# Performance work log

Measured on AMD Instinct MI355X. Metric: run time of the kernel, lower is better.

Reference implementation:

```python
import jax, jax.numpy as jnp
import numpy as np
from jax import lax

B = 128      # graphs per batch
N = 68       # facial landmarks (num_nodes per graph)
C = 3        # input channels
P = 32       # PATCH_SIZE
K = 16       # NUM_KERNELS
FD = 64      # feature_dim
GH = 128     # gcn_hidden_dim
OUT = 2      # output_dim
EG = 8 * N   # edges per graph
T = B * N    # total nodes


def setup_inputs() -> dict:
    key = jax.random.key(0)
    ks = jax.random.split(key, 8)
    x = jax.random.normal(ks[0], (T, C, P, P), jnp.float32)
    e = jax.random.randint(ks[1], (2, B, EG), 0, N)
    offs = (jnp.arange(B) * N)[None, :, None]
    edge_index = (e + offs).reshape(2, -1)            # within-graph edges, global ids
    batch = jnp.repeat(jnp.arange(B), N)              # node -> graph id
    conv_w = jax.random.normal(ks[2], (N, K, C, 3, 3), jnp.float32) * 0.05
    conv_b = jnp.zeros((N, K), jnp.float32)
    lin1_w = jax.random.normal(ks[3], (N, K * (P // 2) * (P // 2), FD), jnp.float32) * 0.02
    lin1_b = jnp.zeros((N, FD), jnp.float32)
    gcn_w = jax.random.normal(ks[4], (FD, GH), jnp.float32) * 0.1
    gcn_b = jnp.zeros((GH,), jnp.float32)
    mlp_w1 = jax.random.normal(ks[5], (GH, GH // 2), jnp.float32) * 0.1
    mlp_b1 = jnp.zeros((GH // 2,), jnp.float32)
    mlp_w2 = jax.random.normal(ks[6], (GH // 2, OUT), jnp.float32) * 0.1
    mlp_b2 = jnp.zeros((OUT,), jnp.float32)
    return dict(x=x, edge_index=edge_index, batch=batch, conv_w=conv_w, conv_b=conv_b,
                lin1_w=lin1_w, lin1_b=lin1_b, gcn_w=gcn_w, gcn_b=gcn_b,
                mlp_w1=mlp_w1, mlp_b1=mlp_b1, mlp_w2=mlp_w2, mlp_b2=mlp_b2)


def reference(x, edge_index, batch, conv_w, conv_b, lin1_w, lin1_b,
              gcn_w, gcn_b, mlp_w1, mlp_b1, mlp_w2, mlp_b2):
    # --- per-node-type CNN routing (nodes are laid out [graph, local_index]) ---
    xr = x.reshape(B, N, C, P, P)

    def cnn_one(xn, w, b):           # xn: [B,C,P,P]  w: [K,C,3,3]
        y = lax.conv_general_dilated(xn, w, (1, 1), 'SAME',
                                     dimension_numbers=('NCHW', 'OIHW', 'NCHW'))
        return jax.nn.relu(y + b[None, :, None, None])

    a = jax.vmap(cnn_one, in_axes=(1, 0, 0), out_axes=1)(xr, conv_w, conv_b)  # [B,N,K,P,P]
    pooled = lax.reduce_window(a, -jnp.inf, lax.max,
                               (1, 1, 1, 2, 2), (1, 1, 1, 2, 2), 'VALID')     # [B,N,K,P/2,P/2]
    flat = pooled.reshape(B, N, -1)
    feats = jax.nn.relu(jnp.einsum('bnf,nfo->bno', flat, lin1_w) + lin1_b[None])  # [B,N,FD]
    nodes = feats.reshape(T, FD)

    # --- GCNConv: add self-loops, symmetric normalization ---
    loop = jnp.arange(T)
    src = jnp.concatenate([edge_index[0], loop])
    dst = jnp.concatenate([edge_index[1], loop])
    deg = jax.ops.segment_sum(jnp.ones_like(dst, jnp.float32), dst, T)
    dis = jnp.where(deg > 0, 1.0 / jnp.sqrt(deg), 0.0)
    norm = dis[src] * dis[dst]
    xw = nodes @ gcn_w                                   # [T,GH]
    h = jax.ops.segment_sum(norm[:, None] * xw[src], dst, T) + gcn_b
    h = jax.nn.relu(h)

    # --- global mean pool over graphs ---
    cnt = jax.ops.segment_sum(jnp.ones((T,), jnp.float32), batch, B)
    g = jax.ops.segment_sum(h, batch, B) / cnt[:, None]  # [B,GH]

    # --- MLP head ---
    z = jax.nn.relu(g @ mlp_w1 + mlp_b1)
    return z @ mlp_w2 + mlp_b2                           # [B,OUT]
```

## Files before the change

### kernel.cpp

```cpp
#include <hip/hip_runtime.h>
#include <hip/hip_fp16.h>

#define B_   128
#define N_   68
#define C_   3
#define P_   32
#define K_   16
#define FD_  64
#define GH_  128
#define EG_  544
#define T_   8704
#define FLAT_ 4096
#define FCH_ 16

typedef __attribute__((ext_vector_type(8))) _Float16 half8;
typedef __attribute__((ext_vector_type(2))) _Float16 half2v;
typedef __attribute__((ext_vector_type(4))) float   floatx4;
typedef __attribute__((ext_vector_type(4))) unsigned int uint32x4;

#define XPITCH 1164

__global__ __launch_bounds__(256) void conv_pool_kernel(
    const float* __restrict__ x, const float* __restrict__ conv_w,
    const float* __restrict__ conv_b, _Float16* __restrict__ pooled) {
  const int t = blockIdx.x;
  const int n = t % N_;
  const int tid = threadIdx.x;

  __shared__ _Float16 xsh[3 * XPITCH];
  __shared__ __align__(16) _Float16 wAS[2][16][32];
  __shared__ __align__(16) _Float16 wCS[2][16][32];
  __shared__ __align__(16) float bS[16];

  const float* wp = conv_w + (size_t)n * (K_ * 27);

  for (int i = tid; i < 1024; i += 256) {
    int sx = i >> 9, k = (i >> 5) & 15, slot = i & 31;
    int q = slot >> 3, r = (slot >> 2) & 1, col = slot & 3;
    int cr = q * 2 + r, c = cr / 3, dy = cr - c * 3, dx = col - sx;
    float v = (dx >= 0 && dx < 3) ? wp[k * 27 + c * 9 + dy * 3 + dx] : 0.0f;
    wAS[sx][k][slot] = (_Float16)v;
  }
  for (int i = tid; i < 1024; i += 256) {
    int sx = i >> 9, k = (i >> 5) & 15, slot = i & 31;
    int q = slot >> 3, j = slot & 7;
    float v = 0.0f;
    if (q == 0 && j < 4) {
      int dx = j - sx;
      if (dx >= 0 && dx < 3) v = wp[k * 27 + 2 * 9 + 2 * 3 + dx];
    }
    wCS[sx][k][slot] = (_Float16)v;
  }
  if (tid < 16) bS[tid] = conv_b[(size_t)n * K_ + tid];

  for (int i = tid; i < 396; i += 256) {
    int c = i / 132, j = i - c * 132;
    int off;
    if (j < 34)       off = j;
    else if (j < 68)  off = 33 * 34 + (j - 34);
    else if (j < 100) off = (j - 68 + 1) * 34;
    else              off = (j - 100 + 1) * 34 + 33;
    xsh[c * XPITCH + off] = (_Float16)0.0f;
  }
  const float4* xg = (const float4*)(x + (size_t)t * (C_ * P_ * P_));
  #pragma unroll
  for (int j = 0; j < 3; j++) {
    int i4 = tid + j * 256;
    float4 v = xg[i4];
    int f0 = i4 * 4;
    int c = f0 >> 10, rem = f0 & 1023, y = rem >> 5, xc = rem & 31;
    _Float16* dp = &xsh[c * XPITCH + (y + 1) * 34 + xc + 1];
    dp[0] = (_Float16)v.x; dp[1] = (_Float16)v.y;
    dp[2] = (_Float16)v.z; dp[3] = (_Float16)v.w;
  }
  __syncthreads();

  const int lane = tid & 63, wave = tid >> 6;
  const int lr = lane & 15, q = lane >> 4;
  const int ldy = lr >> 3, ldx = lr & 7;

  half8 aMain0 = *(const half8*)&wAS[0][lr][q * 8];
  half8 aMain1 = *(const half8*)&wAS[1][lr][q * 8];
  half8 aCorr0 = *(const half8*)&wCS[0][lr][q * 8];
  half8 aCorr1 = *(const half8*)&wCS[1][lr][q * 8];
  floatx4 cbias = *(const floatx4*)&bS[q * 4];

  const int crL = q * 2, crH = crL + 1;
  const int cL = crL / 3, dyL = crL - cL * 3;
  const int cH = crH / 3, dyH = crH - cH * 3;
  const _Float16* chL = &xsh[cL * XPITCH + dyL * 34];
  const _Float16* chH = &xsh[cH * XPITCH + dyH * 34];
  const _Float16* chC = &xsh[2 * XPITCH + 2 * 34];

  #pragma unroll
  for (int i = 0; i < 4; i++) {
    const int qq = wave * 4 + i;
    const int py0 = (qq >> 1) * 2, px0 = (qq & 1) * 8;
    const int py = py0 + ldy, px = px0 + ldx;
    const int ebase = py * 68 + px * 2;
    const _Float16* pL = chL + ebase;
    const _Float16* pH = chH + ebase;
    const _Float16* pC = chC + ebase;

    floatx4 mx;
    #pragma unroll
    for (int sy = 0; sy < 2; sy++) {
      unsigned int uL0 = *(const unsigned int*)&pL[sy * 34];
      unsigned int uL1 = *(const unsigned int*)&pL[sy * 34 + 2];
      unsigned int uH0 = *(const unsigned int*)&pH[sy * 34];
      unsigned int uH1 = *(const unsigned int*)&pH[sy * 34 + 2];
      unsigned int uC0 = *(const unsigned int*)&pC[sy * 34];
      unsigned int uC1 = *(const unsigned int*)&pC[sy * 34 + 2];
      half8 bMain = __builtin_bit_cast(half8, (uint32x4){uL0, uL1, uH0, uH1});
      half8 bCorr = __builtin_bit_cast(half8, (uint32x4){uC0, uC1, uC0, uC1});
      floatx4 d0 = __builtin_amdgcn_mfma_f32_16x16x32_f16(aCorr0, bCorr, cbias, 0, 0, 0);
      d0 = __builtin_amdgcn_mfma_f32_16x16x32_f16(aMain0, bMain, d0, 0, 0, 0);
      floatx4 d1 = __builtin_amdgcn_mfma_f32_16x16x32_f16(aCorr1, bCorr, cbias, 0, 0, 0);
      d1 = __builtin_amdgcn_mfma_f32_16x16x32_f16(aMain1, bMain, d1, 0, 0, 0);
      floatx4 m;
      m[0] = fmaxf(d0[0], d1[0]); m[1] = fmaxf(d0[1], d1[1]);
      m[2] = fmaxf(d0[2], d1[2]); m[3] = fmaxf(d0[3], d1[3]);
      if (sy == 0) mx = m;
      else {
        mx[0] = fmaxf(mx[0], m[0]); mx[1] = fmaxf(mx[1], m[1]);
        mx[2] = fmaxf(mx[2], m[2]); mx[3] = fmaxf(mx[3], m[3]);
      }
    }
    _Float16* op = pooled + (size_t)t * FLAT_ + q * 1024 + py * 16 + px;
    op[0]   = (_Float16)fmaxf(mx[0], 0.0f);
    op[256] = (_Float16)fmaxf(mx[1], 0.0f);
    op[512] = (_Float16)fmaxf(mx[2], 0.0f);
    op[768] = (_Float16)fmaxf(mx[3], 0.0f);
  }
}

__global__ __launch_bounds__(256) void lin1_mfma_kernel(
    const _Float16* __restrict__ pooled, const float* __restrict__ lin1_w,
    float* __restrict__ part) {
  const int n   = blockIdx.x >> 4;
  const int fc  = blockIdx.x & 15;
  const int tid = threadIdx.x;
  const int wave = tid >> 6, lane = tid & 63;
  const int q = lane >> 4, lr = lane & 15;

  __shared__ __align__(16) _Float16 As[128 * 72];
  __shared__ __align__(16) _Float16 Bt[64 * 72];

  floatx4 acc[2][4];
  #pragma unroll
  for (int mt = 0; mt < 2; mt++)
    #pragma unroll
    for (int nt = 0; nt < 4; nt++)
      acc[mt][nt] = (floatx4){0.f, 0.f, 0.f, 0.f};

  const int f_base = fc * 256;
  for (int step = 0; step < 4; step++) {
    const int f0 = f_base + step * 64;

    #pragma unroll
    for (int j = 0; j < 4; j++) {
      int idx = tid + j * 256;
      int r = idx >> 3, ch = idx & 7;
      uint4 v = *(const uint4*)&pooled[(size_t)(r * N_ + n) * FLAT_ + f0 + ch * 8];
      *(uint4*)&As[r * 72 + ch * 8] = v;
    }
    const float* wg = &lin1_w[(size_t)n * (FLAT_ * FD_) + (size_t)f0 * FD_];
    #pragma unroll
    for (int it = 0; it < 2; it++) {
      int p = tid + it * 256;
      int o0 = (p & 15) * 4, k0 = (p >> 4) * 2;
      const float* wgk = wg + k0 * 64 + o0;
      float4 va = *(const float4*)wgk;
      float4 vb = *(const float4*)(wgk + 64);
      *(half2v*)&Bt[(o0 + 0) * 72 + k0] = (half2v){(_Float16)va.x, (_Float16)vb.x};
      *(half2v*)&Bt[(o0 + 1) * 72 + k0] = (half2v){(_Float16)va.y, (_Float16)vb.y};
      *(half2v*)&Bt[(o0 + 2) * 72 + k0] = (half2v){(_Float16)va.z, (_Float16)vb.z};
      *(half2v*)&Bt[(o0 + 3) * 72 + k0] = (half2v){(_Float16)va.w, (_Float16)vb.w};
    }
    __syncthreads();

    #pragma unroll
    for (int kh = 0; kh < 2; kh++) {
      half8 af[2], bf[4];
      #pragma unroll
      for (int mt = 0; mt < 2; mt++)
        af[mt] = *(const half8*)&As[(wave * 32 + mt * 16 + lr) * 72 + kh * 32 + q * 8];
      #pragma unroll
      for (int nt = 0; nt < 4; nt++)
        bf[nt] = *(const half8*)&Bt[(nt * 16 + lr) * 72 + kh * 32 + q * 8];
      #pragma unroll
      for (int mt = 0; mt < 2; mt++)
        #pragma unroll
        for (int nt = 0; nt < 4; nt++)
          acc[mt][nt] = __builtin_amdgcn_mfma_f32_16x16x32_f16(
              af[mt], bf[nt], acc[mt][nt], 0, 0, 0);
    }
    __syncthreads();
  }

  float* pb = part + (size_t)fc * T_ * FD_;
  #pragma unroll
  for (int mt = 0; mt < 2; mt++) {
    #pragma unroll
    for (int v = 0; v < 4; v++) {
      int r = wave * 32 + mt * 16 + q * 4 + v;
      size_t base = (size_t)(r * N_ + n) * FD_;
      #pragma unroll
      for (int nt = 0; nt < 4; nt++)
        pb[base + nt * 16 + lr] = acc[mt][nt][v];
    }
  }
}

__global__ __launch_bounds__(256) void feats_kernel(
    const float* __restrict__ part, const float* __restrict__ lin1_b,
    float* __restrict__ feats) {
  int gid = blockIdx.x * 256 + threadIdx.x;
  int t = gid >> 4, f4 = (gid & 15) * 4;
  int n = t % N_;
  float4 s = *(const float4*)&lin1_b[n * FD_ + f4];
  #pragma unroll
  for (int fc = 0; fc < FCH_; fc++) {
    float4 v = *(const float4*)&part[((size_t)fc * T_ + t) * FD_ + f4];
    s.x += v.x; s.y += v.y; s.z += v.z; s.w += v.w;
  }
  s.x = fmaxf(s.x, 0.f); s.y = fmaxf(s.y, 0.f);
  s.z = fmaxf(s.z, 0.f); s.w = fmaxf(s.w, 0.f);
  *(float4*)&feats[(size_t)t * FD_ + f4] = s;
}

__global__ __launch_bounds__(256) void gcn_agg_kernel(
    const float* __restrict__ feats, const int* __restrict__ edge_index,
    float* __restrict__ agg) {
  const int b  = blockIdx.x >> 1;
  const int fh = blockIdx.x & 1;
  const int tid = threadIdx.x;

  __shared__ float fS[N_ * 33], aS[N_ * 33];
  __shared__ int   esrcS[EG_], edstS[EG_];
  __shared__ float nrmS[EG_];
  __shared__ int   degS[N_];
  __shared__ float disS[N_];

  if (tid < N_) degS[tid] = 0;
  const int* srcp = edge_index;
  const int* dstp = edge_index + (B_ * EG_);
  const int e0 = b * EG_, nbase = b * N_;
  for (int e = tid; e < EG_; e += 256) {
    esrcS[e] = srcp[e0 + e] - nbase;
    edstS[e] = dstp[e0 + e] - nbase;
  }
  for (int idx = tid; idx < N_ * 32; idx += 256) {
    int i = idx >> 5, f = idx & 31;
    fS[i * 33 + f] = feats[(size_t)(b * N_ + i) * FD_ + fh * 32 + f];
  }
  __syncthreads();
  for (int e = tid; e < EG_; e += 256) atomicAdd(&degS[edstS[e]], 1);
  __syncthreads();
  if (tid < N_) disS[tid] = rsqrtf((float)(degS[tid] + 1));
  __syncthreads();
  for (int e = tid; e < EG_; e += 256)
    nrmS[e] = disS[esrcS[e]] * disS[edstS[e]];
  for (int idx = tid; idx < N_ * 32; idx += 256) {
    int i = idx >> 5, f = idx & 31;
    float d = disS[i];
    aS[i * 33 + f] = d * d * fS[i * 33 + f];
  }
  __syncthreads();
  for (int idx = tid; idx < EG_ * 32; idx += 256) {
    int e = idx >> 5, f = idx & 31;
    atomicAdd(&aS[edstS[e] * 33 + f], nrmS[e] * fS[esrcS[e] * 33 + f]);
  }
  __syncthreads();
  for (int idx = tid; idx < N_ * 32; idx += 256) {
    int i = idx >> 5, f = idx & 31;
    agg[(size_t)(b * N_ + i) * FD_ + fh * 32 + f] = aS[i * 33 + f];
  }
}

__global__ __launch_bounds__(512) void gcn_head_kernel(
    const float* __restrict__ agg, const float* __restrict__ gcn_w,
    const float* __restrict__ gcn_b, const float* __restrict__ w1,
    const float* __restrict__ b1, const float* __restrict__ w2,
    const float* __restrict__ b2, float* __restrict__ out) {
  const int b = blockIdx.x;
  const int tid = threadIdx.x;

  __shared__ float aS[N_ * 68];
  __shared__ float wS[FD_ * GH_];
  __shared__ float gP[4][GH_];
  __shared__ float z1S[64];

  for (int i4 = tid; i4 < N_ * 16; i4 += 512) {
    int i = i4 >> 4, qf = (i4 & 15) * 4;
    *(float4*)&aS[i * 68 + qf] = *(const float4*)&agg[(size_t)(b * N_ + i) * FD_ + qf];
  }
  #pragma unroll
  for (int j = 0; j < 4; j++)
    ((float4*)wS)[tid + j * 512] = ((const float4*)gcn_w)[tid + j * 512];
  __syncthreads();

  const int j = tid & 127, ig = tid >> 7;
  float wc[64];
  #pragma unroll
  for (int k = 0; k < 64; k++) wc[k] = wS[k * GH_ + j];
  const float bias = gcn_b[j];
  float gsum = 0.f;
  for (int i = ig; i < N_; i += 4) {
    float acc = bias;
    #pragma unroll
    for (int kq = 0; kq < 16; kq++) {
      float4 a = *(const float4*)&aS[i * 68 + kq * 4];
      acc += a.x * wc[kq * 4] + a.y * wc[kq * 4 + 1]
           + a.z * wc[kq * 4 + 2] + a.w * wc[kq * 4 + 3];
    }
    gsum += fmaxf(acc, 0.f);
  }
  gP[ig][j] = gsum;
  __syncthreads();
  if (tid < GH_)
    gP[0][tid] = (gP[0][tid] + gP[1][tid] + gP[2][tid] + gP[3][tid]) * (1.f / 68.f);
  __syncthreads();
  if (tid < 64) {
    float s = b1[tid];
    #pragma unroll 8
    for (int jj = 0; jj < GH_; jj++) s += gP[0][jj] * w1[jj * 64 + tid];
    z1S[tid] = fmaxf(s, 0.f);
  }
  __syncthreads();
  if (tid < 2) {
    float s = b2[tid];
    #pragma unroll 8
    for (int jj = 0; jj < 64; jj++) s += z1S[jj] * w2[jj * 2 + tid];
    out[b * 2 + tid] = s;
  }
}

extern "C" void kernel_launch(void* const* d_in, const int* in_sizes, int n_in,
                              void* d_out, int out_size, void* d_ws, size_t ws_size,
                              hipStream_t stream) {
  const float* x        = (const float*)d_in[0];
  const int*   edge_idx = (const int*)d_in[1];
  const float* conv_w   = (const float*)d_in[3];
  const float* conv_b   = (const float*)d_in[4];
  const float* lin1_w   = (const float*)d_in[5];
  const float* lin1_b   = (const float*)d_in[6];
  const float* gcn_w    = (const float*)d_in[7];
  const float* gcn_b    = (const float*)d_in[8];
  const float* mlp_w1   = (const float*)d_in[9];
  const float* mlp_b1   = (const float*)d_in[10];
  const float* mlp_w2   = (const float*)d_in[11];
  const float* mlp_b2   = (const float*)d_in[12];
  float* outp = (float*)d_out;

  char* wsb = (char*)d_ws;
  _Float16* pooled = (_Float16*)wsb;
  float* part  = (float*)(wsb + (size_t)T_ * FLAT_ * 2);
  float* feats = part + (size_t)FCH_ * T_ * FD_;
  float* agg   = feats + (size_t)T_ * FD_;

  conv_pool_kernel<<<T_, 256, 0, stream>>>(x, conv_w, conv_b, pooled);
  lin1_mfma_kernel<<<N_ * FCH_, 256, 0, stream>>>(pooled, lin1_w, part);
  feats_kernel<<<544, 256, 0, stream>>>(part, lin1_b, feats);
  gcn_agg_kernel<<<B_ * 2, 256, 0, stream>>>(feats, edge_idx, agg);
  gcn_head_kernel<<<B_, 512, 0, stream>>>(agg, gcn_w, gcn_b,
                                          mlp_w1, mlp_b1, mlp_w2, mlp_b2, outp);
}
```

Measured before the change: 315.3 us.

## Precompute conv weight fragments once per node type and pad LDS rows

```diff
diff --git a/kernel.cpp b/kernel.cpp
--- a/kernel.cpp
+++ b/kernel.cpp
@@ -18,86 +18,94 @@
 typedef __attribute__((ext_vector_type(4))) float   floatx4;
 typedef __attribute__((ext_vector_type(4))) unsigned int uint32x4;
 
-#define XPITCH 1164
+#define ROWP 40
+#define CHP  1400
+
+__global__ __launch_bounds__(256) void wfrag_prep_kernel(
+    const float* __restrict__ conv_w, _Float16* __restrict__ wfrag) {
+  const int n = blockIdx.x;
+  const int tid = threadIdx.x;
+  const float* wp = conv_w + (size_t)n * (K_ * 27);
+  _Float16* out = wfrag + (size_t)n * 2048;
+  for (int i = tid; i < 2048; i += 256) {
+    int sx   = (i >> 10) & 1;
+    int type = (i >> 9) & 1;
+    int k    = (i >> 5) & 15;
+    int slot = i & 31;
+    float v = 0.0f;
+    if (type == 0) {
+      int q = slot >> 3, r = (slot >> 2) & 1, col = slot & 3;
+      int cr = q * 2 + r, c = cr / 3, dy = cr - c * 3, dx = col - sx;
+      if (dx >= 0 && dx < 3) v = wp[k * 27 + c * 9 + dy * 3 + dx];
+    } else {
+      int q = slot >> 3, j = slot & 7;
+      if (q == 0 && j < 4) {
+        int dx = j - sx;
+        if (dx >= 0 && dx < 3) v = wp[k * 27 + 24 + dx];
+      }
+    }
+    out[i] = (_Float16)v;
+  }
+}
 
 __global__ __launch_bounds__(256) void conv_pool_kernel(
-    const float* __restrict__ x, const float* __restrict__ conv_w,
+    const float* __restrict__ x, const _Float16* __restrict__ wfrag,
     const float* __restrict__ conv_b, _Float16* __restrict__ pooled) {
   const int t = blockIdx.x;
   const int n = t % N_;
   const int tid = threadIdx.x;
 
-  __shared__ _Float16 xsh[3 * XPITCH];
-  __shared__ __align__(16) _Float16 wAS[2][16][32];
-  __shared__ __align__(16) _Float16 wCS[2][16][32];
-  __shared__ __align__(16) float bS[16];
-
-  const float* wp = conv_w + (size_t)n * (K_ * 27);
-
-  for (int i = tid; i < 1024; i += 256) {
-    int sx = i >> 9, k = (i >> 5) & 15, slot = i & 31;
-    int q = slot >> 3, r = (slot >> 2) & 1, col = slot & 3;
-    int cr = q * 2 + r, c = cr / 3, dy = cr - c * 3, dx = col - sx;
-    float v = (dx >= 0 && dx < 3) ? wp[k * 27 + c * 9 + dy * 3 + dx] : 0.0f;
-    wAS[sx][k][slot] = (_Float16)v;
-  }
-  for (int i = tid; i < 1024; i += 256) {
-    int sx = i >> 9, k = (i >> 5) & 15, slot = i & 31;
-    int q = slot >> 3, j = slot & 7;
-    float v = 0.0f;
-    if (q == 0 && j < 4) {
-      int dx = j - sx;
-      if (dx >= 0 && dx < 3) v = wp[k * 27 + 2 * 9 + 2 * 3 + dx];
-    }
-    wCS[sx][k][slot] = (_Float16)v;
-  }
-  if (tid < 16) bS[tid] = conv_b[(size_t)n * K_ + tid];
+  __shared__ _Float16 xsh[3 * CHP];
+
+  const int lane = tid & 63;
+  const int lr = lane & 15, q = lane >> 4;
+  const int wave = tid >> 6;
+  const int ldy = lr >> 3, ldx = lr & 7;
+
+  const float4* xg = (const float4*)(x + (size_t)t * (C_ * P_ * P_));
+  float4 xv[3];
+  #pragma unroll
+  for (int j = 0; j < 3; j++) xv[j] = xg[tid + j * 256];
+
+  const _Float16* wf = wfrag + (size_t)n * 2048 + lr * 32 + q * 8;
+  half8 aMain0 = *(const half8*)&wf[0 * 512];
+  half8 aCorr0 = *(const half8*)&wf[1 * 512];
+  half8 aMain1 = *(const half8*)&wf[2 * 512];
+  half8 aCorr1 = *(const half8*)&wf[3 * 512];
+  floatx4 cbias = *(const floatx4*)&conv_b[(size_t)n * K_ + q * 4];
 
   for (int i = tid; i < 396; i += 256) {
     int c = i / 132, j = i - c * 132;
     int off;
     if (j < 34)       off = j;
-    else if (j < 68)  off = 33 * 34 + (j - 34);
-    else if (j < 100) off = (j - 68 + 1) * 34;
-    else              off = (j - 100 + 1) * 34 + 33;
-    xsh[c * XPITCH + off] = (_Float16)0.0f;
-  }
-  const float4* xg = (const float4*)(x + (size_t)t * (C_ * P_ * P_));
+    else if (j < 68)  off = 33 * ROWP + (j - 34);
+    else if (j < 100) off = (j - 68 + 1) * ROWP;
+    else              off = (j - 100 + 1) * ROWP + 33;
+    xsh[c * CHP + off] = (_Float16)0.0f;
+  }
   #pragma unroll
   for (int j = 0; j < 3; j++) {
-    int i4 = tid + j * 256;
-    float4 v = xg[i4];
-    int f0 = i4 * 4;
+    int f0 = (tid + j * 256) * 4;
     int c = f0 >> 10, rem = f0 & 1023, y = rem >> 5, xc = rem & 31;
-    _Float16* dp = &xsh[c * XPITCH + (y + 1) * 34 + xc + 1];
-    dp[0] = (_Float16)v.x; dp[1] = (_Float16)v.y;
-    dp[2] = (_Float16)v.z; dp[3] = (_Float16)v.w;
-  }
-  __syncthreads();
-
-  const int lane = tid & 63, wave = tid >> 6;
-  const int lr = lane & 15, q = lane >> 4;
-  const int ldy = lr >> 3, ldx = lr & 7;
-
-  half8 aMain0 = *(const half8*)&wAS[0][lr][q * 8];
-  half8 aMain1 = *(const half8*)&wAS[1][lr][q * 8];
-  half8 aCorr0 = *(const half8*)&wCS[0][lr][q * 8];
-  half8 aCorr1 = *(const half8*)&wCS[1][lr][q * 8];
-  floatx4 cbias = *(const floatx4*)&bS[q * 4];
+    _Float16* dp = &xsh[c * CHP + (y + 1) * ROWP + xc + 1];
+    dp[0] = (_Float16)xv[j].x; dp[1] = (_Float16)xv[j].y;
+    dp[2] = (_Float16)xv[j].z; dp[3] = (_Float16)xv[j].w;
+  }
+  __syncthreads();
 
   const int crL = q * 2, crH = crL + 1;
   const int cL = crL / 3, dyL = crL - cL * 3;
   const int cH = crH / 3, dyH = crH - cH * 3;
-  const _Float16* chL = &xsh[cL * XPITCH + dyL * 34];
-  const _Float16* chH = &xsh[cH * XPITCH + dyH * 34];
-  const _Float16* chC = &xsh[2 * XPITCH + 2 * 34];
+  const _Float16* chL = &xsh[cL * CHP + dyL * ROWP];
+  const _Float16* chH = &xsh[cH * CHP + dyH * ROWP];
+  const _Float16* chC = &xsh[2 * CHP + 2 * ROWP];
 
   #pragma unroll
   for (int i = 0; i < 4; i++) {
     const int qq = wave * 4 + i;
     const int py0 = (qq >> 1) * 2, px0 = (qq & 1) * 8;
     const int py = py0 + ldy, px = px0 + ldx;
-    const int ebase = py * 68 + px * 2;
+    const int ebase = py * (2 * ROWP) + px * 2;
     const _Float16* pL = chL + ebase;
     const _Float16* pH = chH + ebase;
     const _Float16* pC = chC + ebase;
@@ -105,12 +113,12 @@
     floatx4 mx;
     #pragma unroll
     for (int sy = 0; sy < 2; sy++) {
-      unsigned int uL0 = *(const unsigned int*)&pL[sy * 34];
-      unsigned int uL1 = *(const unsigned int*)&pL[sy * 34 + 2];
-      unsigned int uH0 = *(const unsigned int*)&pH[sy * 34];
-      unsigned int uH1 = *(const unsigned int*)&pH[sy * 34 + 2];
-      unsigned int uC0 = *(const unsigned int*)&pC[sy * 34];
-      unsigned int uC1 = *(const unsigned int*)&pC[sy * 34 + 2];
+      unsigned int uL0 = *(const unsigned int*)&pL[sy * ROWP];
+      unsigned int uL1 = *(const unsigned int*)&pL[sy * ROWP + 2];
+      unsigned int uH0 = *(const unsigned int*)&pH[sy * ROWP];
+      unsigned int uH1 = *(const unsigned int*)&pH[sy * ROWP + 2];
+      unsigned int uC0 = *(const unsigned int*)&pC[sy * ROWP];
+      unsigned int uC1 = *(const unsigned int*)&pC[sy * ROWP + 2];
       half8 bMain = __builtin_bit_cast(half8, (uint32x4){uL0, uL1, uH0, uH1});
       half8 bCorr = __builtin_bit_cast(half8, (uint32x4){uC0, uC1, uC0, uC1});
       floatx4 d0 = __builtin_amdgcn_mfma_f32_16x16x32_f16(aCorr0, bCorr, cbias, 0, 0, 0);
@@ -358,8 +366,10 @@
   float* part  = (float*)(wsb + (size_t)T_ * FLAT_ * 2);
   float* feats = part + (size_t)FCH_ * T_ * FD_;
   float* agg   = feats + (size_t)T_ * FD_;
-
-  conv_pool_kernel<<<T_, 256, 0, stream>>>(x, conv_w, conv_b, pooled);
+  _Float16* wfrag = (_Float16*)(agg + (size_t)T_ * FD_);
+
+  wfrag_prep_kernel<<<N_, 256, 0, stream>>>(conv_w, wfrag);
+  conv_pool_kernel<<<T_, 256, 0, stream>>>(x, wfrag, conv_b, pooled);
   lin1_mfma_kernel<<<N_ * FCH_, 256, 0, stream>>>(pooled, lin1_w, part);
   feats_kernel<<<544, 256, 0, stream>>>(part, lin1_b, feats);
   gcn_agg_kernel<<<B_ * 2, 256, 0, stream>>>(feats, edge_idx, agg);
```

New measurement: 311.8 us. No clear change (-1.1%).
